# Kernel tuning notes

Measured on AMD Instinct MI355X. Metric: run time of the kernel, lower is better.

Reference implementation:

```python
import jax, jax.numpy as jnp
import numpy as np

B, S, E = 4, 2048, 1024


def setup_inputs() -> dict:
    key = jax.random.key(0)
    ks = jax.random.split(key, 7)
    s = 1.0 / np.sqrt(E)  # torch Linear default init scale (uniform bound)
    inp = {
        "input": jax.random.normal(ks[0], (B, S, E), dtype=jnp.float32),
        "masked": 1,
        "W_q": jax.random.uniform(ks[1], (E, E), jnp.float32, -s, s),
        "b_q": jax.random.uniform(ks[2], (E,), jnp.float32, -s, s),
        "W_k": jax.random.uniform(ks[3], (E, E), jnp.float32, -s, s),
        "b_k": jax.random.uniform(ks[4], (E,), jnp.float32, -s, s),
        "W_v": jax.random.uniform(ks[5], (E, E), jnp.float32, -s, s),
        "b_v": jax.random.uniform(ks[6], (E,), jnp.float32, -s, s),
    }
    return inp


def reference(input, masked, W_q, b_q, W_k, b_k, W_v, b_v):
    # torch.nn.Linear: y = x @ W.T + b
    q = jnp.einsum("bse,fe->bsf", input, W_q) + b_q
    k = jnp.einsum("bse,fe->bsf", input, W_k) + b_k
    v = jnp.einsum("bse,fe->bsf", input, W_v) + b_v
    d = q.shape[-1]
    scores = jnp.einsum("bqd,bkd->bqk", q, k) / jnp.sqrt(jnp.float32(d))
    if masked:
        Sq = scores.shape[1]
        causal = jnp.tril(jnp.ones((Sq, Sq), dtype=bool))  # [S,S], broadcast over batch
        scores = jnp.where(causal, scores, -jnp.inf)
    attn = jax.nn.softmax(scores, axis=-1)
    return jnp.einsum("bqk,bkd->bqd", attn, v)
```

## Files before the change

kernel.cpp:

```cpp
#include <hip/hip_runtime.h>

typedef _Float16 f16;
typedef f16 f16x8 __attribute__((ext_vector_type(8)));
typedef f16 f16x4v __attribute__((ext_vector_type(4)));
typedef f16 f16x2v __attribute__((ext_vector_type(2)));
typedef float f32x4 __attribute__((ext_vector_type(4)));

__device__ __forceinline__ void async_ld16(const void* g, void* l) {
    __builtin_amdgcn_global_load_lds(
        (const __attribute__((address_space(1))) unsigned int*)g,
        (__attribute__((address_space(3))) unsigned int*)l, 16, 0, 0);
}

#define VMC(n) asm volatile("s_waitcnt vmcnt(" #n ")" ::: "memory")
#define BAR __builtin_amdgcn_s_barrier()


#define SSTG_A(b, kh, tOff) do {                                                \
    char* d_ = (char*)smem + (b) * 32768 + (kh) * 8192 + stgBase;               \
    async_ld16(pA  + (tOff) * 64 + (kh) * 32, d_);                              \
    async_ld16(pA1 + (tOff) * 64 + (kh) * 32, d_ + 4096);                       \
} while (0)
#define SSTG_B(b, kh, tOff) do {                                                \
    char* d_ = (char*)smem + (b) * 32768 + 16384 + (kh) * 8192 + stgBase;       \
    async_ld16(pB  + (tOff) * 64 + (kh) * 32, d_);                              \
    async_ld16(pB1 + (tOff) * 64 + (kh) * 32, d_ + 4096);                       \
} while (0)
#define SRD(b, kk) do {                                                         \
    const char* sa_ = (const char*)smem + (b) * 32768 + (kk) * 8192 + aOff;     \
    _Pragma("unroll") for (int m_ = 0; m_ < 4; ++m_)                            \
        af[m_] = *(const f16x8*)(sa_ + m_ * 1024);                              \
    const char* sb_ = (const char*)smem + (b) * 32768 + 16384 + (kk) * 8192 + bOff; \
    _Pragma("unroll") for (int n_ = 0; n_ < 4; ++n_)                            \
        bf[n_] = *(const f16x8*)(sb_ + n_ * 1024);                              \
} while (0)
#define SFENCE do {                                                             \
    __builtin_amdgcn_s_barrier();                                               \
    asm volatile("s_waitcnt lgkmcnt(0)" ::: "memory");                          \
    __builtin_amdgcn_sched_barrier(0);                                          \
    __builtin_amdgcn_s_setprio(1);                                              \
    _Pragma("unroll") for (int m_ = 0; m_ < 4; ++m_)                            \
        _Pragma("unroll") for (int n_ = 0; n_ < 4; ++n_)                        \
            acc[m_][n_] = __builtin_amdgcn_mfma_f32_16x16x32_f16(af[m_], bf[n_], acc[m_][n_], 0, 0, 0); \
    __builtin_amdgcn_s_setprio(0);                                              \
} while (0)

__global__ __launch_bounds__(256, 2) void scores128(
    const f16* __restrict__ Q, const f16* __restrict__ K,
    f16* __restrict__ P, const int* __restrict__ maskedp)
{
    const int masked = *maskedp;
    const int bx = blockIdx.x, by = blockIdx.y, bz = blockIdx.z;
    if (masked && bx > by) return;
    const int mBase = by * 128, nBase = bx * 128;
    const bool diag = (masked != 0) && (bx == by);

    __shared__ __align__(16) f16 smem[32768];
    const int tid = threadIdx.x;
    const int wave = tid >> 6, lane = tid & 63;
    const int wrow = wave >> 1, wcol = wave & 1;
    const int quad = lane >> 4, l16 = lane & 15;
    const int rowLane = tid >> 2;
    const int cOff = ((tid & 3) ^ ((tid >> 3) & 3)) * 8;
    const int stgBase = wave * 1024;
    const int swz  = (quad ^ ((l16 >> 1) & 3)) * 16;
    const int aOff = (wrow * 64 + l16) * 64 + swz;
    const int bOff = (wcol * 64 + l16) * 64 + swz;

    const f16* Ab = Q + (long)bz * (2048L * 1024);
    const f16* Bb = K + (long)bz * (2048L * 1024);
    const f16* pA  = Ab + (long)(mBase + rowLane) * 1024 + cOff;
    const f16* pA1 = pA + 64 * 1024;
    const f16* pB  = Bb + (long)(nBase + rowLane) * 1024 + cOff;
    const f16* pB1 = pB + 64 * 1024;

    f32x4 acc[4][4];
#pragma unroll
    for (int m = 0; m < 4; ++m)
#pragma unroll
        for (int n = 0; n < 4; ++n) acc[m][n] = (f32x4){0.f, 0.f, 0.f, 0.f};
    f16x8 af[4], bf[4];

    SSTG_A(0, 0, 0); SSTG_B(0, 0, 0);
    SSTG_A(0, 1, 0); SSTG_B(0, 1, 0);
    SSTG_A(1, 0, 1); SSTG_B(1, 0, 1);
    VMC(4);
    BAR;

#pragma unroll 1
    for (int i = 0; i < 7; ++i) {
        SRD(0, 0); SSTG_A(1, 1, 1); SSTG_B(1, 1, 1);
        SFENCE; VMC(8); BAR;
        SRD(0, 1); SSTG_A(0, 0, 2); SSTG_B(0, 0, 2);
        SFENCE; VMC(8); BAR;
        SRD(1, 0); SSTG_A(0, 1, 2); SSTG_B(0, 1, 2);
        SFENCE; VMC(8); BAR;
        SRD(1, 1); SSTG_A(1, 0, 3); SSTG_B(1, 0, 3);
        SFENCE; VMC(8); BAR;
        pA += 128; pA1 += 128; pB += 128; pB1 += 128;
    }
    SRD(0, 0); SSTG_A(1, 1, 1); SSTG_B(1, 1, 1);
    SFENCE; VMC(8); BAR;
    SRD(0, 1);
    SFENCE; VMC(4); BAR;
    SRD(1, 0);
    SFENCE; VMC(0); BAR;
    SRD(1, 1);
    SFENCE;

    f16* Crow = P + (long)bz * (2048L * 2048);
#pragma unroll
    for (int m = 0; m < 4; ++m)
#pragma unroll
        for (int n = 0; n < 4; ++n)
#pragma unroll
            for (int r = 0; r < 4; ++r) {
                const int row = mBase + wrow * 64 + m * 16 + quad * 4 + r;
                const int col = nBase + wcol * 64 + n * 16 + l16;
                float e = __expf(acc[m][n][r] * 0.03125f);
                if (diag && col > row) e = 0.f;
                Crow[(long)row * 2048 + col] = (f16)e;
            }
}

#undef SSTG_A
#undef SSTG_B
#undef SRD
#undef SFENCE

#define QSTG(j, o) do {                                                         \
    char* da_ = (char*)smem + (j) * 24576 + wave * 1024;                        \
    async_ld16(pA  + (o) * 32, da_);                                            \
    char* db_ = (char*)smem + (j) * 24576 + 8192 + wave * 1024;                 \
    async_ld16(pB  + (o) * 32, db_);                                            \
    async_ld16(pB1 + (o) * 32, db_ + 8192);                                     \
} while (0)
#define QRD(j) do {                                                             \
    const char* sa_ = (const char*)smem + (j) * 24576 + aOff;                   \
    _Pragma("unroll") for (int m_ = 0; m_ < 4; ++m_)                            \
        af[m_] = *(const f16x8*)(sa_ + m_ * 1024);                              \
    const char* sb_ = (const char*)smem + (j) * 24576 + 8192 + bOff;            \
    _Pragma("unroll") for (int n_ = 0; n_ < 4; ++n_)                            \
        bf[n_] = *(const f16x8*)(sb_ + n_ * 1024);                              \
} while (0)
#define QFENCE do {                                                             \
    __builtin_amdgcn_s_barrier();                                               \
    asm volatile("s_waitcnt lgkmcnt(0)" ::: "memory");                          \
    __builtin_amdgcn_sched_barrier(0);                                          \
    __builtin_amdgcn_s_setprio(1);                                              \
    _Pragma("unroll") for (int m_ = 0; m_ < 4; ++m_)                            \
        _Pragma("unroll") for (int n_ = 0; n_ < 4; ++n_)                        \
            acc[m_][n_] = __builtin_amdgcn_mfma_f32_16x16x32_f16(af[m_], bf[n_], acc[m_][n_], 0, 0, 0); \
    __builtin_amdgcn_s_setprio(0);                                              \
} while (0)
#define QT(j, j2, o2) do { QRD(j); QSTG(j2, o2); QFENCE; VMC(3); BAR; } while (0)

__global__ __launch_bounds__(512, 2) void qkv128(
    const f16* __restrict__ A, const f16* __restrict__ Bt,
    const float* __restrict__ b_q, const float* __restrict__ b_k,
    const float* __restrict__ b_v,
    f16* __restrict__ Q16, f16* __restrict__ K16, f16* __restrict__ Vt16)
{
    const int orig = blockIdx.x;
    const int xcd = orig & 7;
    const int s = orig >> 3;
    const int by = xcd * 8 + (s & 7);
    const int bx = s >> 3;
    const int mBase = by * 128, nBase = bx * 256;

    __shared__ __align__(16) f16 smem[36864];
    const int tid = threadIdx.x;
    const int wave = tid >> 6, lane = tid & 63;
    const int wrow = wave >> 2, wcol = wave & 3;
    const int quad = lane >> 4, l16 = lane & 15;
    const int rowLane = tid >> 2;
    const int cOff = ((tid & 3) ^ ((tid >> 3) & 3)) * 8;
    const int swz  = (quad ^ ((l16 >> 1) & 3)) * 16;
    const int aOff = (wrow * 64 + l16) * 64 + swz;
    const int bOff = (wcol * 64 + l16) * 64 + swz;

    const f16* pA  = A  + (long)(mBase + rowLane) * 1024 + cOff;
    const f16* pB  = Bt + (long)(nBase + rowLane) * 1024 + cOff;
    const f16* pB1 = pB + 128 * 1024;

    f32x4 acc[4][4];
#pragma unroll
    for (int m = 0; m < 4; ++m)
#pragma unroll
        for (int n = 0; n < 4; ++n) acc[m][n] = (f32x4){0.f, 0.f, 0.f, 0.f};
    f16x8 af[4], bf[4];

    QSTG(0, 0); QSTG(1, 1);
    VMC(3);
    BAR;

#pragma unroll 1
    for (int g = 0; g < 10; ++g) {
        QT(0, 2, 2);
        QT(1, 0, 3);
        QT(2, 1, 4);
        pA += 96; pB += 96; pB1 += 96;
    }
    QRD(0); QFENCE; VMC(0); BAR;
    QRD(1); QFENCE;
    BAR;

    const int seg = nBase >> 10;
    const float* bs = (seg == 0) ? b_q : (seg == 1) ? b_k : b_v;
    const int lcb = (nBase & 1023) + wcol * 64;
    float bvv[4];
#pragma unroll
    for (int n = 0; n < 4; ++n) bvv[n] = bs[lcb + n * 16 + l16];

    if (seg < 2) {
        f16* dst = (seg == 0) ? Q16 : K16;
#pragma unroll
        for (int m = 0; m < 4; ++m)
#pragma unroll
            for (int n = 0; n < 4; ++n)
#pragma unroll
                for (int r = 0; r < 4; ++r) {
                    const int row = mBase + wrow * 64 + m * 16 + quad * 4 + r;
                    dst[(long)row * 1024 + lcb + n * 16 + l16] =
                        (f16)(acc[m][n][r] + bvv[n]);
                }
    } else {
        const int b = mBase >> 11;
        const int s0 = (mBase & 2047) + wrow * 64;
        const int e0 = (nBase & 1023) + wcol * 64;
        f16* epiW = smem + wave * (64 * 72);
#pragma unroll
        for (int m = 0; m < 4; ++m)
#pragma unroll
            for (int n = 0; n < 4; ++n) {
                f16x4v pk;
#pragma unroll
                for (int r = 0; r < 4; ++r)
                    pk[r] = (f16)(acc[m][n][r] + bvv[n]);
                *(f16x4v*)&epiW[(n * 16 + l16) * 72 + m * 16 + quad * 4] = pk;
            }
        asm volatile("s_waitcnt lgkmcnt(0)" ::: "memory");
#pragma unroll
        for (int it = 0; it < 8; ++it) {
            const int e = it * 8 + (lane >> 3);
            const f16x8 v = *(const f16x8*)&epiW[e * 72 + (lane & 7) * 8];
            *(f16x8*)(Vt16 + ((long)b * 1024 + e0 + e) * 2048 + s0 +
                      (lane & 7) * 8) = v;
        }
    }
}

#undef QSTG
#undef QRD
#undef QFENCE
#undef QT

#if defined(__has_builtin)
#if __has_builtin(__builtin_amdgcn_fdot2)
#define HAVE_FDOT2 1
#endif
#endif

#ifdef HAVE_FDOT2
#define PSUM do {                                                               \
    const f16x2v one_ = {(f16)1, (f16)1};                                       \
    _Pragma("unroll") for (int m_ = 0; m_ < 4; ++m_) {                          \
        const f16x2v* ph_ = (const f16x2v*)&af[m_];                             \
        _Pragma("unroll") for (int j_ = 0; j_ < 4; ++j_)                        \
            rs[m_] = __builtin_amdgcn_fdot2(ph_[j_], one_, rs[m_], false);      \
    }                                                                           \
} while (0)
#else
#define PSUM do {                                                               \
    _Pragma("unroll") for (int m_ = 0; m_ < 4; ++m_)                            \
        _Pragma("unroll") for (int j_ = 0; j_ < 8; ++j_)                        \
            rs[m_] += (float)af[m_][j_];                                        \
} while (0)
#endif

#define PSTG_A(b, kh, tOff) do {                                                \
    char* d_ = (char*)smem + (b) * 32768 + (kh) * 8192 + stgBase;               \
    async_ld16(pA  + (tOff) * 64 + (kh) * 32, d_);                              \
    async_ld16(pA1 + (tOff) * 64 + (kh) * 32, d_ + 4096);                       \
} while (0)
#define PSTG_B(b, kh, tOff) do {                                                \
    char* d_ = (char*)smem + (b) * 32768 + 16384 + (kh) * 8192 + stgBase;       \
    async_ld16(pB  + (tOff) * 64 + (kh) * 32, d_);                              \
    async_ld16(pB1 + (tOff) * 64 + (kh) * 32, d_ + 4096);                       \
} while (0)
#define PRD(b, kk) do {                                                         \
    const char* sa_ = (const char*)smem + (b) * 32768 + (kk) * 8192 + aOff;     \
    _Pragma("unroll") for (int m_ = 0; m_ < 4; ++m_)                            \
        af[m_] = *(const f16x8*)(sa_ + m_ * 1024);                              \
    const char* sb_ = (const char*)smem + (b) * 32768 + 16384 + (kk) * 8192 + bOff; \
    _Pragma("unroll") for (int n_ = 0; n_ < 4; ++n_)                            \
        bf[n_] = *(const f16x8*)(sb_ + n_ * 1024);                              \
} while (0)
#define PFENCE do {                                                             \
    __builtin_amdgcn_s_barrier();                                               \
    asm volatile("s_waitcnt lgkmcnt(0)" ::: "memory");                          \
    __builtin_amdgcn_sched_barrier(0);                                          \
    __builtin_amdgcn_s_setprio(1);                                              \
    _Pragma("unroll") for (int m_ = 0; m_ < 4; ++m_)                            \
        _Pragma("unroll") for (int n_ = 0; n_ < 4; ++n_)                        \
            acc[m_][n_] = __builtin_amdgcn_mfma_f32_16x16x32_f16(af[m_], bf[n_], acc[m_][n_], 0, 0, 0); \
    __builtin_amdgcn_s_setprio(0);                                              \
    PSUM;                                                                       \
} while (0)

__global__ __launch_bounds__(256, 2) void pv128(
    const f16* __restrict__ P, const f16* __restrict__ Vt,
    float* __restrict__ out, const int* __restrict__ maskedp)
{
    const int masked = *maskedp;
    const int bx = blockIdx.x, bz = blockIdx.z;
    const int by = (bz >= 2) ? blockIdx.y : (gridDim.y - 1 - blockIdx.y);
    const int mBase = by * 128, nBase = bx * 128;
    const int nIter = masked ? (by + 1) : 16;

    __shared__ __align__(16) f16 smem[32768];
    const int tid = threadIdx.x;
    const int wave = tid >> 6, lane = tid & 63;
    const int wrow = wave >> 1, wcol = wave & 1;
    const int quad = lane >> 4, l16 = lane & 15;
    const int rowLane = tid >> 2;
    const int cOff = ((tid & 3) ^ ((tid >> 3) & 3)) * 8;
    const int stgBase = wave * 1024;
    const int swz  = (quad ^ ((l16 >> 1) & 3)) * 16;
    const int aOff = (wrow * 64 + l16) * 64 + swz;
    const int bOff = (wcol * 64 + l16) * 64 + swz;

    const f16* Pb = P  + (long)bz * (2048L * 2048);
    const f16* Vb = Vt + (long)bz * (1024L * 2048);
    const f16* pA  = Pb + (long)(mBase + rowLane) * 2048 + cOff;
    const f16* pA1 = pA + 64 * 2048;
    const f16* pB  = Vb + (long)(nBase + rowLane) * 2048 + cOff;
    const f16* pB1 = pB + 64 * 2048;

    f32x4 acc[4][4];
#pragma unroll
    for (int m = 0; m < 4; ++m)
#pragma unroll
        for (int n = 0; n < 4; ++n) acc[m][n] = (f32x4){0.f, 0.f, 0.f, 0.f};
    f16x8 af[4], bf[4];
    float rs[4] = {0.f, 0.f, 0.f, 0.f};

    PSTG_A(0, 0, 0); PSTG_B(0, 0, 0);
    PSTG_A(0, 1, 0); PSTG_B(0, 1, 0);
    PSTG_A(1, 0, 1); PSTG_B(1, 0, 1);
    VMC(4);
    BAR;

#pragma unroll 1
    for (int i = 0; i < nIter - 1; ++i) {
        PRD(0, 0); PSTG_A(1, 1, 1); PSTG_B(1, 1, 1);
        PFENCE; VMC(8); BAR;
        PRD(0, 1); PSTG_A(0, 0, 2); PSTG_B(0, 0, 2);
        PFENCE; VMC(8); BAR;
        PRD(1, 0); PSTG_A(0, 1, 2); PSTG_B(0, 1, 2);
        PFENCE; VMC(8); BAR;
        PRD(1, 1); PSTG_A(1, 0, 3); PSTG_B(1, 0, 3);
        PFENCE; VMC(8); BAR;
        pA += 128; pA1 += 128; pB += 128; pB1 += 128;
    }
    PRD(0, 0); PSTG_A(1, 1, 1); PSTG_B(1, 1, 1);
    PFENCE; VMC(8); BAR;
    PRD(0, 1);
    PFENCE; VMC(4); BAR;
    PRD(1, 0);
    PFENCE; VMC(0); BAR;
    PRD(1, 1);
    PFENCE;

#pragma unroll
    for (int m = 0; m < 4; ++m) {
        rs[m] += __shfl_xor(rs[m], 16);
        rs[m] += __shfl_xor(rs[m], 32);
    }

    float* ob = out + (long)bz * (2048L * 1024);
#pragma unroll
    for (int m = 0; m < 4; ++m)
#pragma unroll
        for (int r = 0; r < 4; ++r) {
            const int row = mBase + wrow * 64 + m * 16 + quad * 4 + r;
            const float inv = 1.f / __shfl(rs[m], quad * 4 + r);
#pragma unroll
            for (int n = 0; n < 4; ++n) {
                const int col = nBase + wcol * 64 + n * 16 + l16;
                ob[(long)row * 1024 + col] = acc[m][n][r] * inv;
            }
        }
}

#undef PSTG_A
#undef PSTG_B
#undef PRD
#undef PFENCE
#undef PSUM
#undef VMC
#undef BAR

__global__ void cvt_all(const float* __restrict__ inp,
                        const float* __restrict__ W0,
                        const float* __restrict__ W1,
                        const float* __restrict__ W2,
                        f16* __restrict__ inp16, f16* __restrict__ W3)
{
    const int bxx = blockIdx.x;
    const float* src;
    f16* dst;
    int i;
    if (bxx < 8192) {
        src = inp; dst = inp16;
        i = bxx * 256 + threadIdx.x;
    } else {
        const int wb = bxx - 8192;
        const int which = wb >> 10;
        src = (which == 0) ? W0 : (which == 1) ? W1 : W2;
        dst = W3 + (long)which * 1024 * 1024;
        i = (wb & 1023) * 256 + threadIdx.x;
    }
    const float4 v = ((const float4*)src)[i];
    f16x4v o;
    o[0] = (f16)v.x; o[1] = (f16)v.y; o[2] = (f16)v.z; o[3] = (f16)v.w;
    ((f16x4v*)dst)[i] = o;
}

extern "C" void kernel_launch(void* const* d_in, const int* in_sizes, int n_in,
                              void* d_out, int out_size, void* d_ws, size_t ws_size,
                              hipStream_t stream)
{
    const float* inp = (const float*)d_in[0];
    const int* masked = (const int*)d_in[1];
    const float* Wq = (const float*)d_in[2];
    const float* bq = (const float*)d_in[3];
    const float* Wk = (const float*)d_in[4];
    const float* bk = (const float*)d_in[5];
    const float* Wv = (const float*)d_in[6];
    const float* bv = (const float*)d_in[7];
    float* out = (float*)d_out;

    const int S = 2048, E = 1024;
    const long nTok = (long)4 * S;

    char* ws = (char*)d_ws;
    f16* inp16 = (f16*)ws;   ws += nTok * E * 2;
    f16* W3    = (f16*)ws;   ws += (long)3 * E * E * 2;
    f16* Q16   = (f16*)ws;   ws += nTok * E * 2;
    f16* K16   = (f16*)ws;   ws += nTok * E * 2;
    f16* Vt16  = (f16*)ws;   ws += nTok * E * 2;
    f16* P16   = (f16*)ws;   ws += (long)4 * S * S * 2;

    cvt_all<<<dim3(8192 + 3072), dim3(256), 0, stream>>>(
        inp, Wq, Wk, Wv, inp16, W3);

    qkv128<<<dim3(768), dim3(512), 0, stream>>>(
        inp16, W3, bq, bk, bv, Q16, K16, Vt16);

    scores128<<<dim3(16, 16, 4), dim3(256), 0, stream>>>(
        Q16, K16, P16, masked);

    pv128<<<dim3(8, 16, 4), dim3(256), 0, stream>>>(
        P16, Vt16, out, masked);
}
```

Baseline: 233.0 us.

## Halve QKV GEMM block to 4 waves, each computing a 128x64 tile

```diff
diff --git a/kernel.cpp b/kernel.cpp
--- a/kernel.cpp
+++ b/kernel.cpp
@@ -130,14 +130,17 @@
 
 #define QSTG(j, o) do {                                                         \
     char* da_ = (char*)smem + (j) * 24576 + wave * 1024;                        \
-    async_ld16(pA  + (o) * 32, da_);                                            \
+    async_ld16(pA0 + (o) * 32, da_);                                            \
+    async_ld16(pA1 + (o) * 32, da_ + 4096);                                     \
     char* db_ = (char*)smem + (j) * 24576 + 8192 + wave * 1024;                 \
-    async_ld16(pB  + (o) * 32, db_);                                            \
-    async_ld16(pB1 + (o) * 32, db_ + 8192);                                     \
+    async_ld16(pB0 + (o) * 32, db_);                                            \
+    async_ld16(pB1 + (o) * 32, db_ + 4096);                                     \
+    async_ld16(pB2 + (o) * 32, db_ + 8192);                                     \
+    async_ld16(pB3 + (o) * 32, db_ + 12288);                                    \
 } while (0)
 #define QRD(j) do {                                                             \
     const char* sa_ = (const char*)smem + (j) * 24576 + aOff;                   \
-    _Pragma("unroll") for (int m_ = 0; m_ < 4; ++m_)                            \
+    _Pragma("unroll") for (int m_ = 0; m_ < 8; ++m_)                            \
         af[m_] = *(const f16x8*)(sa_ + m_ * 1024);                              \
     const char* sb_ = (const char*)smem + (j) * 24576 + 8192 + bOff;            \
     _Pragma("unroll") for (int n_ = 0; n_ < 4; ++n_)                            \
@@ -148,14 +151,14 @@
     asm volatile("s_waitcnt lgkmcnt(0)" ::: "memory");                          \
     __builtin_amdgcn_sched_barrier(0);                                          \
     __builtin_amdgcn_s_setprio(1);                                              \
-    _Pragma("unroll") for (int m_ = 0; m_ < 4; ++m_)                            \
+    _Pragma("unroll") for (int m_ = 0; m_ < 8; ++m_)                            \
         _Pragma("unroll") for (int n_ = 0; n_ < 4; ++n_)                        \
             acc[m_][n_] = __builtin_amdgcn_mfma_f32_16x16x32_f16(af[m_], bf[n_], acc[m_][n_], 0, 0, 0); \
     __builtin_amdgcn_s_setprio(0);                                              \
 } while (0)
-#define QT(j, j2, o2) do { QRD(j); QSTG(j2, o2); QFENCE; VMC(3); BAR; } while (0)
-
-__global__ __launch_bounds__(512, 2) void qkv128(
+#define QT(j, j2, o2) do { QRD(j); QSTG(j2, o2); QFENCE; VMC(6); BAR; } while (0)
+
+__global__ __launch_bounds__(256, 2) void qkv128(
     const f16* __restrict__ A, const f16* __restrict__ Bt,
     const float* __restrict__ b_q, const float* __restrict__ b_k,
     const float* __restrict__ b_v,
@@ -171,27 +174,29 @@
     __shared__ __align__(16) f16 smem[36864];
     const int tid = threadIdx.x;
     const int wave = tid >> 6, lane = tid & 63;
-    const int wrow = wave >> 2, wcol = wave & 3;
     const int quad = lane >> 4, l16 = lane & 15;
     const int rowLane = tid >> 2;
     const int cOff = ((tid & 3) ^ ((tid >> 3) & 3)) * 8;
     const int swz  = (quad ^ ((l16 >> 1) & 3)) * 16;
-    const int aOff = (wrow * 64 + l16) * 64 + swz;
-    const int bOff = (wcol * 64 + l16) * 64 + swz;
-
-    const f16* pA  = A  + (long)(mBase + rowLane) * 1024 + cOff;
-    const f16* pB  = Bt + (long)(nBase + rowLane) * 1024 + cOff;
-    const f16* pB1 = pB + 128 * 1024;
-
-    f32x4 acc[4][4];
-#pragma unroll
-    for (int m = 0; m < 4; ++m)
+    const int aOff = l16 * 64 + swz;
+    const int bOff = (wave * 64 + l16) * 64 + swz;
+
+    const f16* pA0 = A  + (long)(mBase + rowLane) * 1024 + cOff;
+    const f16* pA1 = pA0 + 64 * 1024;
+    const f16* pB0 = Bt + (long)(nBase + rowLane) * 1024 + cOff;
+    const f16* pB1 = pB0 + 64 * 1024;
+    const f16* pB2 = pB0 + 128 * 1024;
+    const f16* pB3 = pB0 + 192 * 1024;
+
+    f32x4 acc[8][4];
+#pragma unroll
+    for (int m = 0; m < 8; ++m)
 #pragma unroll
         for (int n = 0; n < 4; ++n) acc[m][n] = (f32x4){0.f, 0.f, 0.f, 0.f};
-    f16x8 af[4], bf[4];
+    f16x8 af[8], bf[4];
 
     QSTG(0, 0); QSTG(1, 1);
-    VMC(3);
+    VMC(6);
     BAR;
 
 #pragma unroll 1
@@ -199,7 +204,7 @@
         QT(0, 2, 2);
         QT(1, 0, 3);
         QT(2, 1, 4);
-        pA += 96; pB += 96; pB1 += 96;
+        pA0 += 96; pA1 += 96; pB0 += 96; pB1 += 96; pB2 += 96; pB3 += 96;
     }
     QRD(0); QFENCE; VMC(0); BAR;
     QRD(1); QFENCE;
@@ -207,7 +212,7 @@
 
     const int seg = nBase >> 10;
     const float* bs = (seg == 0) ? b_q : (seg == 1) ? b_k : b_v;
-    const int lcb = (nBase & 1023) + wcol * 64;
+    const int lcb = (nBase & 1023) + wave * 64;
     float bvv[4];
 #pragma unroll
     for (int n = 0; n < 4; ++n) bvv[n] = bs[lcb + n * 16 + l16];
@@ -215,37 +220,37 @@
     if (seg < 2) {
         f16* dst = (seg == 0) ? Q16 : K16;
 #pragma unroll
-        for (int m = 0; m < 4; ++m)
+        for (int m = 0; m < 8; ++m)
 #pragma unroll
             for (int n = 0; n < 4; ++n)
 #pragma unroll
                 for (int r = 0; r < 4; ++r) {
-                    const int row = mBase + wrow * 64 + m * 16 + quad * 4 + r;
+                    const int row = mBase + m * 16 + quad * 4 + r;
                     dst[(long)row * 1024 + lcb + n * 16 + l16] =
                         (f16)(acc[m][n][r] + bvv[n]);
                 }
     } else {
         const int b = mBase >> 11;
-        const int s0 = (mBase & 2047) + wrow * 64;
-        const int e0 = (nBase & 1023) + wcol * 64;
-        f16* epiW = smem + wave * (64 * 72);
-#pragma unroll
-        for (int m = 0; m < 4; ++m)
+        const int s0 = mBase & 2047;
+        const int e0 = (nBase & 1023) + wave * 64;
+        f16* epiW = smem + wave * (64 * 136);
+#pragma unroll
+        for (int m = 0; m < 8; ++m)
 #pragma unroll
             for (int n = 0; n < 4; ++n) {
                 f16x4v pk;
 #pragma unroll
                 for (int r = 0; r < 4; ++r)
                     pk[r] = (f16)(acc[m][n][r] + bvv[n]);
-                *(f16x4v*)&epiW[(n * 16 + l16) * 72 + m * 16 + quad * 4] = pk;
+                *(f16x4v*)&epiW[(n * 16 + l16) * 136 + m * 16 + quad * 4] = pk;
             }
         asm volatile("s_waitcnt lgkmcnt(0)" ::: "memory");
 #pragma unroll
-        for (int it = 0; it < 8; ++it) {
-            const int e = it * 8 + (lane >> 3);
-            const f16x8 v = *(const f16x8*)&epiW[e * 72 + (lane & 7) * 8];
+        for (int it = 0; it < 16; ++it) {
+            const int e = it * 4 + (lane >> 4);
+            const f16x8 v = *(const f16x8*)&epiW[e * 136 + (lane & 15) * 8];
             *(f16x8*)(Vt16 + ((long)b * 1024 + e0 + e) * 2048 + s0 +
-                      (lane & 7) * 8) = v;
+                      (lane & 15) * 8) = v;
         }
     }
 }
@@ -455,7 +460,7 @@
     cvt_all<<<dim3(8192 + 3072), dim3(256), 0, stream>>>(
         inp, Wq, Wk, Wv, inp16, W3);
 
-    qkv128<<<dim3(768), dim3(512), 0, stream>>>(
+    qkv128<<<dim3(768), dim3(256), 0, stream>>>(
         inp16, W3, bq, bk, bv, Q16, K16, Vt16);
 
     scores128<<<dim3(16, 16, 4), dim3(256), 0, stream>>>(
```

Result: faster. 220.3 us (-5.5%).
